# Kernel tuning notes

Measured on AMD Instinct MI355X. Metric: run time of the kernel, lower is better.

The kernel has to match this reference:

```python
import jax, jax.numpy as jnp
import numpy as np

TAU = 0.1
EPS = 1e-8  # torch CosineSimilarity eps


def _neg_indices(B):
    # static (numpy) column indices of the non-masked (negative) entries per row
    N = 2 * B
    mask = ~(np.eye(N, dtype=bool)
             | np.eye(N, k=B, dtype=bool)
             | np.eye(N, k=-B, dtype=bool))
    return np.where(mask)[1].reshape(N, N - 2)  # [2B, 2B-2]


def setup_inputs() -> dict:
    key = jax.random.key(0)
    k1, k2 = jax.random.split(key)
    zis = jax.random.normal(k1, (4096, 128), dtype=jnp.float32)
    zjs = jax.random.normal(k2, (4096, 128), dtype=jnp.float32)
    return {"zis": zis, "zjs": zjs}


def reference(zis, zjs):
    B = zis.shape[0]
    N = 2 * B
    reps = jnp.concatenate([zjs, zis], axis=0)  # [2B, D]
    # cosine similarity via normalize + GEMM
    norm = jnp.linalg.norm(reps, axis=-1, keepdims=True)
    rn = reps / jnp.maximum(norm, EPS)
    sim = rn @ rn.T  # [2B, 2B]

    l_pos = jnp.diagonal(sim, offset=B)   # [B]
    r_pos = jnp.diagonal(sim, offset=-B)  # [B]
    positives = jnp.concatenate([l_pos, r_pos])[:, None]  # [2B, 1]

    neg_idx = jnp.asarray(_neg_indices(B))  # static [2B, 2B-2]
    negatives = jnp.take_along_axis(sim, neg_idx, axis=1)  # [2B, 2B-2]

    logits = jnp.concatenate([positives, negatives], axis=1) / TAU  # [2B, 2B-1]
    logp = jax.nn.log_softmax(logits, axis=-1)
    # labels are all zeros; CrossEntropyLoss(reduction='sum')
    CE = -jnp.sum(logp[:, 0])
    # pt = mean over full [2B, 2B-1] of onehot * softmax = sum softmax[:,0] / (2B*(2B-1))
    pt = jnp.sum(jnp.exp(logp[:, 0])) / (N * (N - 1))
    epsilon = float(B)
    loss = CE / N + epsilon * (1.0 / B - pt)
    return loss
```

## Files before the change

kernel.cpp:

```cpp
#include <hip/hip_runtime.h>
#include <hip/hip_bf16.h>

#define BSZ 4096
#define NSZ 8192
#define DD  128
#define TILE 128
#define INV_TAU 10.0f
#define GROUPS 8
#define TPB 8

typedef __attribute__((ext_vector_type(8))) short bf16x8;
typedef __attribute__((ext_vector_type(4))) float f32x4;

typedef __attribute__((address_space(3))) unsigned int lds_u32;
typedef const __attribute__((address_space(1))) unsigned int glb_u32;

__global__ __launch_bounds__(256)
void norm_kernel(const float* __restrict__ zis,
                 const float* __restrict__ zjs,
                 __hip_bfloat16* __restrict__ rn) {
    const int row  = blockIdx.x * 4 + (threadIdx.x >> 6);
    const int lane = threadIdx.x & 63;
    const float* src = (row < BSZ) ? (zjs + (size_t)row * DD)
                                   : (zis + (size_t)(row - BSZ) * DD);
    float2 v = *(const float2*)(src + lane * 2);
    float ss = v.x * v.x + v.y * v.y;
    #pragma unroll
    for (int off = 32; off; off >>= 1) ss += __shfl_xor(ss, off);
    float inv = 1.0f / fmaxf(sqrtf(ss), 1e-8f);
    __hip_bfloat16 a = __float2bfloat16(v.x * inv);
    __hip_bfloat16 b = __float2bfloat16(v.y * inv);
    ushort2 pk;
    pk.x = *(const ushort*)&a;
    pk.y = *(const ushort*)&b;
    *(ushort2*)(rn + (size_t)row * DD + lane * 2) = pk;
}

__global__ __launch_bounds__(256, 2)
void sim_lse_kernel(const __hip_bfloat16* __restrict__ rn,
                    float* __restrict__ partials,
                    float* __restrict__ pos) {
    __shared__ ushort Bt[2][TILE * DD];

    const int g   = blockIdx.x;
    const int bi  = blockIdx.y;
    const int tid = threadIdx.x;
    const int wid  = tid >> 6;
    const int lane = tid & 63;
    const int l15  = lane & 15;
    const int kg   = lane >> 4;
    const int wm   = wid >> 1;
    const int wn   = wid & 1;

    const char* abase = (const char*)rn + (size_t)(bi * TILE + wm * 64 + l15) * 256;
    bf16x8 af[4][4];
    #pragma unroll
    for (int mf = 0; mf < 4; ++mf)
        #pragma unroll
        for (int kk = 0; kk < 4; ++kk)
            af[mf][kk] = *(const bf16x8*)(abase + mf * 16 * 256 + kk * 64 + kg * 16);

    {
        const char* gbase = (const char*)rn + (size_t)(g * TPB) * TILE * 256;
        #pragma unroll
        for (int j = 0; j < 8; ++j) {
            int cs  = (wid * 8 + j) * 64 + lane;
            int gsc = cs ^ ((cs >> 4) & 7);
            __builtin_amdgcn_global_load_lds((glb_u32*)(gbase + (size_t)gsc * 16),
                                             (lds_u32*)(&Bt[0][0] + (wid * 8 + j) * 512),
                                             16, 0, 0);
        }
    }
    __syncthreads();

    float rsum[4][4] = {};
    const int bjp = (bi + 32) & 63;

    for (int t = 0; t < TPB; ++t) {
        const int bj = g * TPB + t;

        if (t + 1 < TPB) {
            const char* gbase = (const char*)rn + (size_t)(bj + 1) * TILE * 256;
            ushort* dst = &Bt[(t + 1) & 1][0];
            #pragma unroll
            for (int j = 0; j < 8; ++j) {
                int cs  = (wid * 8 + j) * 64 + lane;
                int gsc = cs ^ ((cs >> 4) & 7);
                __builtin_amdgcn_global_load_lds((glb_u32*)(gbase + (size_t)gsc * 16),
                                                 (lds_u32*)(dst + (wid * 8 + j) * 512),
                                                 16, 0, 0);
            }
        }

        f32x4 acc[4][4] = {};
        const char* Bb = (const char*)&Bt[t & 1][0];
        #pragma unroll
        for (int kk = 0; kk < 4; ++kk) {
            const int kb = kk * 64 + kg * 16;
            bf16x8 bfr[4];
            #pragma unroll
            for (int nf = 0; nf < 4; ++nf) {
                int cR = wn * 64 + nf * 16 + l15;
                int o = cR * 256 + kb;
                bfr[nf] = *(const bf16x8*)(Bb + (o ^ ((cR & 7) << 4)));
            }
            #pragma unroll
            for (int mf = 0; mf < 4; ++mf)
                #pragma unroll
                for (int nf = 0; nf < 4; ++nf)
                    acc[mf][nf] = __builtin_amdgcn_mfma_f32_16x16x32_bf16(
                        af[mf][kk], bfr[nf], acc[mf][nf], 0, 0, 0);
        }

        const bool diag = (bj == bi);
        const bool posb = (bj == bjp) && (wm == wn);
        const bool dglb = diag && (wm == wn);
        #pragma unroll
        for (int mf = 0; mf < 4; ++mf) {
            #pragma unroll
            for (int nf = 0; nf < 4; ++nf) {
                #pragma unroll
                for (int reg = 0; reg < 4; ++reg) {
                    float s = acc[mf][nf][reg];
                    bool hit = (mf == nf) && ((kg * 4 + reg) == l15);
                    if (posb && hit)
                        pos[bi * TILE + wm * 64 + mf * 16 + l15] = s;
                    float p = __expf(s * INV_TAU);
                    if (dglb && hit) p = 0.0f;
                    rsum[mf][reg] += p;
                }
            }
        }

        __syncthreads();
    }

    #pragma unroll
    for (int mf = 0; mf < 4; ++mf)
        #pragma unroll
        for (int reg = 0; reg < 4; ++reg) {
            float v = rsum[mf][reg];
            v += __shfl_xor(v, 1);
            v += __shfl_xor(v, 2);
            v += __shfl_xor(v, 4);
            v += __shfl_xor(v, 8);
            rsum[mf][reg] = v;
        }

    float* red = (float*)&Bt[0][0];
    if (wn == 1 && l15 == 0) {
        #pragma unroll
        for (int mf = 0; mf < 4; ++mf)
            #pragma unroll
            for (int reg = 0; reg < 4; ++reg)
                red[wm * 64 + mf * 16 + kg * 4 + reg] = rsum[mf][reg];
    }
    __syncthreads();
    if (wn == 0 && l15 == 0) {
        #pragma unroll
        for (int mf = 0; mf < 4; ++mf)
            #pragma unroll
            for (int reg = 0; reg < 4; ++reg) {
                int lr = wm * 64 + mf * 16 + kg * 4 + reg;
                partials[(size_t)g * NSZ + bi * TILE + lr] = rsum[mf][reg] + red[lr];
            }
    }
}

__global__ __launch_bounds__(1024)
void reduce_kernel(const float* __restrict__ partials,
                   const float* __restrict__ pos,
                   float* __restrict__ out) {
    int tid = threadIdx.x;
    int base = tid * 8;
    float se[8] = {0.f, 0.f, 0.f, 0.f, 0.f, 0.f, 0.f, 0.f};
    #pragma unroll
    for (int gr = 0; gr < GROUPS; ++gr) {
        const float* p = partials + (size_t)gr * NSZ + base;
        float4 a = *(const float4*)(p);
        float4 b = *(const float4*)(p + 4);
        se[0] += a.x; se[1] += a.y; se[2] += a.z; se[3] += a.w;
        se[4] += b.x; se[5] += b.y; se[6] += b.z; se[7] += b.w;
    }
    float ce = 0.f, pt = 0.f;
    #pragma unroll
    for (int h = 0; h < 2; ++h) {
        float4 p4 = *(const float4*)(pos + base + h * 4);
        const float* pp = (const float*)&p4;
        #pragma unroll
        for (int q = 0; q < 4; ++q) {
            float s = se[h * 4 + q];
            ce += __logf(s) - pp[q] * INV_TAU;
            pt += __expf(pp[q] * INV_TAU) / s;
        }
    }
    #pragma unroll
    for (int off = 32; off; off >>= 1) {
        ce += __shfl_xor(ce, off);
        pt += __shfl_xor(pt, off);
    }
    __shared__ float lce[16], lpt[16];
    if ((tid & 63) == 0) { lce[tid >> 6] = ce; lpt[tid >> 6] = pt; }
    __syncthreads();
    if (tid == 0) {
        float CE = 0.f, PT = 0.f;
        #pragma unroll
        for (int w = 0; w < 16; ++w) { CE += lce[w]; PT += lpt[w]; }
        float loss = CE / (float)NSZ + 1.0f
                   - PT * ((float)BSZ / ((float)NSZ * (float)(NSZ - 1)));
        out[0] = loss;
    }
}

extern "C" void kernel_launch(void* const* d_in, const int* in_sizes, int n_in,
                              void* d_out, int out_size, void* d_ws, size_t ws_size,
                              hipStream_t stream) {
    const float* zis = (const float*)d_in[0];
    const float* zjs = (const float*)d_in[1];
    float* out = (float*)d_out;

    char* ws = (char*)d_ws;
    __hip_bfloat16* rn = (__hip_bfloat16*)ws;
    float* partials = (float*)(ws + 2 * 1024 * 1024);
    float* pos      = (float*)(ws + 2 * 1024 * 1024 + 256 * 1024);

    norm_kernel<<<NSZ / 4, 256, 0, stream>>>(zis, zjs, rn);

    dim3 grid(GROUPS, 64);
    sim_lse_kernel<<<grid, 256, 0, stream>>>(rn, partials, pos);

    reduce_kernel<<<1, 1024, 0, stream>>>(partials, pos, out);
}
```

Baseline: 40.94 us.

## Load B fragments directly from global memory, dropping LDS double buffering

The similarity kernel no longer stages B tiles through double-buffered LDS with global_load_lds and per-tile barriers. Each wave now reads its B fragments straight from global memory into registers, processing the N dimension in two halves to limit live accumulators, and the 2-blocks-per-CU launch bound is removed. Exponentials switch to exp2f with the 1/tau and log2(e) factors folded into one constant, and the self-similarity term is subtracted afterwards instead of masked per element. This trades the LDS traffic and barriers for duplicated global/L2 reads across waves, which adds some cancellation risk in the diagonal subtraction.

```diff
diff --git a/kernel.cpp b/kernel.cpp
--- a/kernel.cpp
+++ b/kernel.cpp
@@ -5,15 +5,12 @@
 #define NSZ 8192
 #define DD  128
 #define TILE 128
-#define INV_TAU 10.0f
 #define GROUPS 8
 #define TPB 8
+#define C2 14.426950408889634f
 
 typedef __attribute__((ext_vector_type(8))) short bf16x8;
 typedef __attribute__((ext_vector_type(4))) float f32x4;
-
-typedef __attribute__((address_space(3))) unsigned int lds_u32;
-typedef const __attribute__((address_space(1))) unsigned int glb_u32;
 
 __global__ __launch_bounds__(256)
 void norm_kernel(const float* __restrict__ zis,
@@ -36,12 +33,10 @@
     *(ushort2*)(rn + (size_t)row * DD + lane * 2) = pk;
 }
 
-__global__ __launch_bounds__(256, 2)
+__global__ __launch_bounds__(256)
 void sim_lse_kernel(const __hip_bfloat16* __restrict__ rn,
                     float* __restrict__ partials,
                     float* __restrict__ pos) {
-    __shared__ ushort Bt[2][TILE * DD];
-
     const int g   = blockIdx.x;
     const int bi  = blockIdx.y;
     const int tid = threadIdx.x;
@@ -60,81 +55,68 @@
         for (int kk = 0; kk < 4; ++kk)
             af[mf][kk] = *(const bf16x8*)(abase + mf * 16 * 256 + kk * 64 + kg * 16);
 
-    {
-        const char* gbase = (const char*)rn + (size_t)(g * TPB) * TILE * 256;
-        #pragma unroll
-        for (int j = 0; j < 8; ++j) {
-            int cs  = (wid * 8 + j) * 64 + lane;
-            int gsc = cs ^ ((cs >> 4) & 7);
-            __builtin_amdgcn_global_load_lds((glb_u32*)(gbase + (size_t)gsc * 16),
-                                             (lds_u32*)(&Bt[0][0] + (wid * 8 + j) * 512),
-                                             16, 0, 0);
-        }
-    }
-    __syncthreads();
-
     float rsum[4][4] = {};
     const int bjp = (bi + 32) & 63;
 
     for (int t = 0; t < TPB; ++t) {
         const int bj = g * TPB + t;
-
-        if (t + 1 < TPB) {
-            const char* gbase = (const char*)rn + (size_t)(bj + 1) * TILE * 256;
-            ushort* dst = &Bt[(t + 1) & 1][0];
-            #pragma unroll
-            for (int j = 0; j < 8; ++j) {
-                int cs  = (wid * 8 + j) * 64 + lane;
-                int gsc = cs ^ ((cs >> 4) & 7);
-                __builtin_amdgcn_global_load_lds((glb_u32*)(gbase + (size_t)gsc * 16),
-                                                 (lds_u32*)(dst + (wid * 8 + j) * 512),
-                                                 16, 0, 0);
+        const char* bbase = (const char*)rn
+                          + (size_t)bj * TILE * 256 + (size_t)(wn * 64) * 256;
+        const bool dglb = (bj == bi)  && (wm == wn);
+        const bool pglb = (bj == bjp) && (wm == wn);
+
+        #pragma unroll
+        for (int nh = 0; nh < 2; ++nh) {
+            bf16x8 bfr[2][4];
+            #pragma unroll
+            for (int nf2 = 0; nf2 < 2; ++nf2)
+                #pragma unroll
+                for (int kk = 0; kk < 4; ++kk)
+                    bfr[nf2][kk] = *(const bf16x8*)(bbase
+                        + (size_t)((nh * 2 + nf2) * 16 + l15) * 256 + kk * 64 + kg * 16);
+
+            f32x4 acc[4][2] = {};
+            #pragma unroll
+            for (int kk = 0; kk < 4; ++kk)
+                #pragma unroll
+                for (int mf = 0; mf < 4; ++mf)
+                    #pragma unroll
+                    for (int nf2 = 0; nf2 < 2; ++nf2)
+                        acc[mf][nf2] = __builtin_amdgcn_mfma_f32_16x16x32_bf16(
+                            af[mf][kk], bfr[nf2][kk], acc[mf][nf2], 0, 0, 0);
+
+            #pragma unroll
+            for (int mf = 0; mf < 4; ++mf)
+                #pragma unroll
+                for (int nf2 = 0; nf2 < 2; ++nf2)
+                    #pragma unroll
+                    for (int reg = 0; reg < 4; ++reg)
+                        rsum[mf][reg] += exp2f(acc[mf][nf2][reg] * C2);
+
+            if (dglb) {
+                #pragma unroll
+                for (int nf2 = 0; nf2 < 2; ++nf2) {
+                    const int mf = nh * 2 + nf2;
+                    #pragma unroll
+                    for (int reg = 0; reg < 4; ++reg)
+                        if (kg * 4 + reg == l15)
+                            rsum[mf][reg] -= exp2f(acc[mf][nf2][reg] * C2);
+                }
             }
-        }
-
-        f32x4 acc[4][4] = {};
-        const char* Bb = (const char*)&Bt[t & 1][0];
-        #pragma unroll
-        for (int kk = 0; kk < 4; ++kk) {
-            const int kb = kk * 64 + kg * 16;
-            bf16x8 bfr[4];
-            #pragma unroll
-            for (int nf = 0; nf < 4; ++nf) {
-                int cR = wn * 64 + nf * 16 + l15;
-                int o = cR * 256 + kb;
-                bfr[nf] = *(const bf16x8*)(Bb + (o ^ ((cR & 7) << 4)));
-            }
-            #pragma unroll
-            for (int mf = 0; mf < 4; ++mf)
-                #pragma unroll
-                for (int nf = 0; nf < 4; ++nf)
-                    acc[mf][nf] = __builtin_amdgcn_mfma_f32_16x16x32_bf16(
-                        af[mf][kk], bfr[nf], acc[mf][nf], 0, 0, 0);
-        }
-
-        const bool diag = (bj == bi);
-        const bool posb = (bj == bjp) && (wm == wn);
-        const bool dglb = diag && (wm == wn);
-        #pragma unroll
-        for (int mf = 0; mf < 4; ++mf) {
-            #pragma unroll
-            for (int nf = 0; nf < 4; ++nf) {
-                #pragma unroll
-                for (int reg = 0; reg < 4; ++reg) {
-                    float s = acc[mf][nf][reg];
-                    bool hit = (mf == nf) && ((kg * 4 + reg) == l15);
-                    if (posb && hit)
-                        pos[bi * TILE + wm * 64 + mf * 16 + l15] = s;
-                    float p = __expf(s * INV_TAU);
-                    if (dglb && hit) p = 0.0f;
-                    rsum[mf][reg] += p;
+            if (pglb) {
+                #pragma unroll
+                for (int nf2 = 0; nf2 < 2; ++nf2) {
+                    const int mf = nh * 2 + nf2;
+                    #pragma unroll
+                    for (int reg = 0; reg < 4; ++reg)
+                        if (kg * 4 + reg == l15)
+                            pos[bi * TILE + wm * 64 + mf * 16 + l15] = acc[mf][nf2][reg];
                 }
             }
         }
-
-        __syncthreads();
-    }
-
+    }
+
+    __shared__ float red[2][64];
     #pragma unroll
     for (int mf = 0; mf < 4; ++mf)
         #pragma unroll
@@ -146,14 +128,12 @@
             v += __shfl_xor(v, 8);
             rsum[mf][reg] = v;
         }
-
-    float* red = (float*)&Bt[0][0];
     if (wn == 1 && l15 == 0) {
         #pragma unroll
         for (int mf = 0; mf < 4; ++mf)
             #pragma unroll
             for (int reg = 0; reg < 4; ++reg)
-                red[wm * 64 + mf * 16 + kg * 4 + reg] = rsum[mf][reg];
+                red[wm][mf * 16 + kg * 4 + reg] = rsum[mf][reg];
     }
     __syncthreads();
     if (wn == 0 && l15 == 0) {
@@ -161,8 +141,9 @@
         for (int mf = 0; mf < 4; ++mf)
             #pragma unroll
             for (int reg = 0; reg < 4; ++reg) {
-                int lr = wm * 64 + mf * 16 + kg * 4 + reg;
-                partials[(size_t)g * NSZ + bi * TILE + lr] = rsum[mf][reg] + red[lr];
+                int lr = mf * 16 + kg * 4 + reg;
+                partials[(size_t)g * NSZ + bi * TILE + wm * 64 + lr] =
+                    rsum[mf][reg] + red[wm][lr];
             }
     }
 }
@@ -190,8 +171,8 @@
         #pragma unroll
         for (int q = 0; q < 4; ++q) {
             float s = se[h * 4 + q];
-            ce += __logf(s) - pp[q] * INV_TAU;
-            pt += __expf(pp[q] * INV_TAU) / s;
+            ce += __logf(s) - pp[q] * 10.0f;
+            pt += exp2f(pp[q] * C2) / s;
         }
     }
     #pragma unroll
```

Result: slower. 51.64 us (+26.1%).

## Exploit symmetry of similarity matrix to compute only half the tiles

Applied to the files above, without the earlier changes.

Uses the symmetry of the cosine-similarity matrix so each block computes only tile offsets 0..31 (plus offset 32 for half the rows), emitting both row sums and column sums per tile. Column partial sums go into extra partial buffers that the reduce kernel now sums over 70-72 slices. This roughly halves the MFMA and exp work in the main kernel. In exchange the reduce kernel reads much more data and runs as a single block, and each tile now does extra cross-lane shuffles and column-sum writes.

```diff
diff --git a/kernel.cpp b/kernel.cpp
--- a/kernel.cpp
+++ b/kernel.cpp
@@ -5,9 +5,6 @@
 #define NSZ 8192
 #define DD  128
 #define TILE 128
-#define INV_TAU 10.0f
-#define GROUPS 8
-#define TPB 8
 
 typedef __attribute__((ext_vector_type(8))) short bf16x8;
 typedef __attribute__((ext_vector_type(4))) float f32x4;
@@ -42,7 +39,7 @@
                     float* __restrict__ pos) {
     __shared__ ushort Bt[2][TILE * DD];
 
-    const int g   = blockIdx.x;
+    const int q   = blockIdx.x;
     const int bi  = blockIdx.y;
     const int tid = threadIdx.x;
     const int wid  = tid >> 6;
@@ -52,6 +49,8 @@
     const int wm   = wid >> 1;
     const int wn   = wid & 1;
 
+    const int nt = (bi < 32 && (bi & 7) == q) ? 5 : 4;
+
     const char* abase = (const char*)rn + (size_t)(bi * TILE + wm * 64 + l15) * 256;
     bf16x8 af[4][4];
     #pragma unroll
@@ -61,7 +60,7 @@
             af[mf][kk] = *(const bf16x8*)(abase + mf * 16 * 256 + kk * 64 + kg * 16);
 
     {
-        const char* gbase = (const char*)rn + (size_t)(g * TPB) * TILE * 256;
+        const char* gbase = (const char*)rn + (size_t)(((bi + q * 4) & 63)) * TILE * 256;
         #pragma unroll
         for (int j = 0; j < 8; ++j) {
             int cs  = (wid * 8 + j) * 64 + lane;
@@ -74,13 +73,15 @@
     __syncthreads();
 
     float rsum[4][4] = {};
-    const int bjp = (bi + 32) & 63;
-
-    for (int t = 0; t < TPB; ++t) {
-        const int bj = g * TPB + t;
-
-        if (t + 1 < TPB) {
-            const char* gbase = (const char*)rn + (size_t)(bj + 1) * TILE * 256;
+
+    for (int t = 0; t < nt; ++t) {
+        const int d  = (t < 4) ? q * 4 + t : 32;
+        const int bj = (bi + d) & 63;
+
+        if (t + 1 < nt) {
+            const int dn  = (t + 1 < 4) ? q * 4 + t + 1 : 32;
+            const int bjn = (bi + dn) & 63;
+            const char* gbase = (const char*)rn + (size_t)bjn * TILE * 256;
             ushort* dst = &Bt[(t + 1) & 1][0];
             #pragma unroll
             for (int j = 0; j < 8; ++j) {
@@ -112,9 +113,9 @@
                         af[mf][kk], bfr[nf], acc[mf][nf], 0, 0, 0);
         }
 
-        const bool diag = (bj == bi);
-        const bool posb = (bj == bjp) && (wm == wn);
-        const bool dglb = diag && (wm == wn);
+        const bool dglb = (d == 0)  && (wm == wn);
+        const bool pglb = (d == 32) && (wm == wn);
+        float csum[4] = {0.f, 0.f, 0.f, 0.f};
         #pragma unroll
         for (int mf = 0; mf < 4; ++mf) {
             #pragma unroll
@@ -122,13 +123,27 @@
                 #pragma unroll
                 for (int reg = 0; reg < 4; ++reg) {
                     float s = acc[mf][nf][reg];
-                    bool hit = (mf == nf) && ((kg * 4 + reg) == l15);
-                    if (posb && hit)
+                    bool hit = (mf == nf) && (kg * 4 + reg == l15);
+                    if (pglb && hit) {
                         pos[bi * TILE + wm * 64 + mf * 16 + l15] = s;
-                    float p = __expf(s * INV_TAU);
+                        pos[(bi + 32) * TILE + wm * 64 + mf * 16 + l15] = s;
+                    }
+                    float p = __expf(s * 10.0f);
                     if (dglb && hit) p = 0.0f;
                     rsum[mf][reg] += p;
+                    csum[nf] += p;
                 }
+            }
+        }
+
+        if (d != 0) {
+            float* cp = partials + (size_t)(8 + (d - 1) * 2 + wm) * NSZ + bj * TILE;
+            #pragma unroll
+            for (int nf = 0; nf < 4; ++nf) {
+                float v = csum[nf];
+                v += __shfl_xor(v, 16);
+                v += __shfl_xor(v, 32);
+                if (kg == 0) cp[wn * 64 + nf * 16 + l15] = v;
             }
         }
 
@@ -162,7 +177,7 @@
             #pragma unroll
             for (int reg = 0; reg < 4; ++reg) {
                 int lr = wm * 64 + mf * 16 + kg * 4 + reg;
-                partials[(size_t)g * NSZ + bi * TILE + lr] = rsum[mf][reg] + red[lr];
+                partials[(size_t)q * NSZ + bi * TILE + lr] = rsum[mf][reg] + red[lr];
             }
     }
 }
@@ -174,24 +189,33 @@
     int tid = threadIdx.x;
     int base = tid * 8;
     float se[8] = {0.f, 0.f, 0.f, 0.f, 0.f, 0.f, 0.f, 0.f};
-    #pragma unroll
-    for (int gr = 0; gr < GROUPS; ++gr) {
+    for (int gr = 0; gr < 70; ++gr) {
         const float* p = partials + (size_t)gr * NSZ + base;
         float4 a = *(const float4*)(p);
         float4 b = *(const float4*)(p + 4);
         se[0] += a.x; se[1] += a.y; se[2] += a.z; se[3] += a.w;
         se[4] += b.x; se[5] += b.y; se[6] += b.z; se[7] += b.w;
     }
+    if (base >= BSZ) {
+        #pragma unroll
+        for (int gr = 70; gr < 72; ++gr) {
+            const float* p = partials + (size_t)gr * NSZ + base;
+            float4 a = *(const float4*)(p);
+            float4 b = *(const float4*)(p + 4);
+            se[0] += a.x; se[1] += a.y; se[2] += a.z; se[3] += a.w;
+            se[4] += b.x; se[5] += b.y; se[6] += b.z; se[7] += b.w;
+        }
+    }
     float ce = 0.f, pt = 0.f;
     #pragma unroll
     for (int h = 0; h < 2; ++h) {
         float4 p4 = *(const float4*)(pos + base + h * 4);
         const float* pp = (const float*)&p4;
         #pragma unroll
-        for (int q = 0; q < 4; ++q) {
-            float s = se[h * 4 + q];
-            ce += __logf(s) - pp[q] * INV_TAU;
-            pt += __expf(pp[q] * INV_TAU) / s;
+        for (int qq = 0; qq < 4; ++qq) {
+            float s = se[h * 4 + qq];
+            ce += __logf(s) - pp[qq] * 10.0f;
+            pt += __expf(pp[qq] * 10.0f) / s;
         }
     }
     #pragma unroll
@@ -222,11 +246,11 @@
     char* ws = (char*)d_ws;
     __hip_bfloat16* rn = (__hip_bfloat16*)ws;
     float* partials = (float*)(ws + 2 * 1024 * 1024);
-    float* pos      = (float*)(ws + 2 * 1024 * 1024 + 256 * 1024);
+    float* pos      = (float*)(ws + 2 * 1024 * 1024 + 72 * NSZ * 4);
 
     norm_kernel<<<NSZ / 4, 256, 0, stream>>>(zis, zjs, rn);
 
-    dim3 grid(GROUPS, 64);
+    dim3 grid(8, 64);
     sim_lse_kernel<<<grid, 256, 0, stream>>>(rn, partials, pos);
 
     reduce_kernel<<<1, 1024, 0, stream>>>(partials, pos, out);
```

After: 86.56 us. +111.4%, slower.

## Use 8 waves per block with 32-row tiles and drop LDS row reduction

Applied to the files above, without the earlier changes.

Moves the similarity/LSE kernel from 256 to 512 threads per block. Each wave now owns a 32x64 output sub-tile instead of 64x64, which halves the register-held A fragments and accumulators and spreads the tile loads over more waves. The cross-wave LDS reduction and its barrier are removed. Each wave instead writes its row sums to a separate partial slot, which doubles the partial buffer and the work in the final reduce kernel. This aims to raise latency hiding and occupancy, at the cost of more partial-buffer traffic and smaller per-wave MFMA work.

```diff
diff --git a/kernel.cpp b/kernel.cpp
--- a/kernel.cpp
+++ b/kernel.cpp
@@ -5,7 +5,6 @@
 #define NSZ 8192
 #define DD  128
 #define TILE 128
-#define INV_TAU 10.0f
 #define GROUPS 8
 #define TPB 8
 
@@ -36,7 +35,7 @@
     *(ushort2*)(rn + (size_t)row * DD + lane * 2) = pk;
 }
 
-__global__ __launch_bounds__(256, 2)
+__global__ __launch_bounds__(512)
 void sim_lse_kernel(const __hip_bfloat16* __restrict__ rn,
                     float* __restrict__ partials,
                     float* __restrict__ pos) {
@@ -52,10 +51,10 @@
     const int wm   = wid >> 1;
     const int wn   = wid & 1;
 
-    const char* abase = (const char*)rn + (size_t)(bi * TILE + wm * 64 + l15) * 256;
-    bf16x8 af[4][4];
-    #pragma unroll
-    for (int mf = 0; mf < 4; ++mf)
+    const char* abase = (const char*)rn + (size_t)(bi * TILE + wm * 32 + l15) * 256;
+    bf16x8 af[2][4];
+    #pragma unroll
+    for (int mf = 0; mf < 2; ++mf)
         #pragma unroll
         for (int kk = 0; kk < 4; ++kk)
             af[mf][kk] = *(const bf16x8*)(abase + mf * 16 * 256 + kk * 64 + kg * 16);
@@ -63,18 +62,20 @@
     {
         const char* gbase = (const char*)rn + (size_t)(g * TPB) * TILE * 256;
         #pragma unroll
-        for (int j = 0; j < 8; ++j) {
-            int cs  = (wid * 8 + j) * 64 + lane;
+        for (int j = 0; j < 4; ++j) {
+            int cs  = (wid * 4 + j) * 64 + lane;
             int gsc = cs ^ ((cs >> 4) & 7);
             __builtin_amdgcn_global_load_lds((glb_u32*)(gbase + (size_t)gsc * 16),
-                                             (lds_u32*)(&Bt[0][0] + (wid * 8 + j) * 512),
+                                             (lds_u32*)(&Bt[0][0] + (wid * 4 + j) * 512),
                                              16, 0, 0);
         }
     }
     __syncthreads();
 
-    float rsum[4][4] = {};
+    float rsum[2][4] = {};
     const int bjp = (bi + 32) & 63;
+    const int nfd = (wm & 1) * 2;
+    const bool wdiag = (wn == (wm >> 1));
 
     for (int t = 0; t < TPB; ++t) {
         const int bj = g * TPB + t;
@@ -83,16 +84,16 @@
             const char* gbase = (const char*)rn + (size_t)(bj + 1) * TILE * 256;
             ushort* dst = &Bt[(t + 1) & 1][0];
             #pragma unroll
-            for (int j = 0; j < 8; ++j) {
-                int cs  = (wid * 8 + j) * 64 + lane;
+            for (int j = 0; j < 4; ++j) {
+                int cs  = (wid * 4 + j) * 64 + lane;
                 int gsc = cs ^ ((cs >> 4) & 7);
                 __builtin_amdgcn_global_load_lds((glb_u32*)(gbase + (size_t)gsc * 16),
-                                                 (lds_u32*)(dst + (wid * 8 + j) * 512),
+                                                 (lds_u32*)(dst + (wid * 4 + j) * 512),
                                                  16, 0, 0);
             }
         }
 
-        f32x4 acc[4][4] = {};
+        f32x4 acc[2][4] = {};
         const char* Bb = (const char*)&Bt[t & 1][0];
         #pragma unroll
         for (int kk = 0; kk < 4; ++kk) {
@@ -105,27 +106,26 @@
                 bfr[nf] = *(const bf16x8*)(Bb + (o ^ ((cR & 7) << 4)));
             }
             #pragma unroll
-            for (int mf = 0; mf < 4; ++mf)
+            for (int mf = 0; mf < 2; ++mf)
                 #pragma unroll
                 for (int nf = 0; nf < 4; ++nf)
                     acc[mf][nf] = __builtin_amdgcn_mfma_f32_16x16x32_bf16(
                         af[mf][kk], bfr[nf], acc[mf][nf], 0, 0, 0);
         }
 
-        const bool diag = (bj == bi);
-        const bool posb = (bj == bjp) && (wm == wn);
-        const bool dglb = diag && (wm == wn);
-        #pragma unroll
-        for (int mf = 0; mf < 4; ++mf) {
+        const bool dglb = (bj == bi)  && wdiag;
+        const bool pglb = (bj == bjp) && wdiag;
+        #pragma unroll
+        for (int mf = 0; mf < 2; ++mf) {
             #pragma unroll
             for (int nf = 0; nf < 4; ++nf) {
                 #pragma unroll
                 for (int reg = 0; reg < 4; ++reg) {
                     float s = acc[mf][nf][reg];
-                    bool hit = (mf == nf) && ((kg * 4 + reg) == l15);
-                    if (posb && hit)
-                        pos[bi * TILE + wm * 64 + mf * 16 + l15] = s;
-                    float p = __expf(s * INV_TAU);
+                    bool hit = (nf == nfd + mf) && (kg * 4 + reg == l15);
+                    if (pglb && hit)
+                        pos[bi * TILE + wm * 32 + mf * 16 + l15] = s;
+                    float p = __expf(s * 10.0f);
                     if (dglb && hit) p = 0.0f;
                     rsum[mf][reg] += p;
                 }
@@ -136,7 +136,7 @@
     }
 
     #pragma unroll
-    for (int mf = 0; mf < 4; ++mf)
+    for (int mf = 0; mf < 2; ++mf)
         #pragma unroll
         for (int reg = 0; reg < 4; ++reg) {
             float v = rsum[mf][reg];
@@ -144,27 +144,10 @@
             v += __shfl_xor(v, 2);
             v += __shfl_xor(v, 4);
             v += __shfl_xor(v, 8);
-            rsum[mf][reg] = v;
-        }
-
-    float* red = (float*)&Bt[0][0];
-    if (wn == 1 && l15 == 0) {
-        #pragma unroll
-        for (int mf = 0; mf < 4; ++mf)
-            #pragma unroll
-            for (int reg = 0; reg < 4; ++reg)
-                red[wm * 64 + mf * 16 + kg * 4 + reg] = rsum[mf][reg];
-    }
-    __syncthreads();
-    if (wn == 0 && l15 == 0) {
-        #pragma unroll
-        for (int mf = 0; mf < 4; ++mf)
-            #pragma unroll
-            for (int reg = 0; reg < 4; ++reg) {
-                int lr = wm * 64 + mf * 16 + kg * 4 + reg;
-                partials[(size_t)g * NSZ + bi * TILE + lr] = rsum[mf][reg] + red[lr];
-            }
-    }
+            if (l15 == 0)
+                partials[(size_t)(g * 2 + wn) * NSZ
+                         + bi * TILE + wm * 32 + mf * 16 + kg * 4 + reg] = v;
+        }
 }
 
 __global__ __launch_bounds__(1024)
@@ -175,7 +158,7 @@
     int base = tid * 8;
     float se[8] = {0.f, 0.f, 0.f, 0.f, 0.f, 0.f, 0.f, 0.f};
     #pragma unroll
-    for (int gr = 0; gr < GROUPS; ++gr) {
+    for (int gr = 0; gr < 2 * GROUPS; ++gr) {
         const float* p = partials + (size_t)gr * NSZ + base;
         float4 a = *(const float4*)(p);
         float4 b = *(const float4*)(p + 4);
@@ -190,8 +173,8 @@
         #pragma unroll
         for (int q = 0; q < 4; ++q) {
             float s = se[h * 4 + q];
-            ce += __logf(s) - pp[q] * INV_TAU;
-            pt += __expf(pp[q] * INV_TAU) / s;
+            ce += __logf(s) - pp[q] * 10.0f;
+            pt += __expf(pp[q] * 10.0f) / s;
         }
     }
     #pragma unroll
@@ -222,12 +205,12 @@
     char* ws = (char*)d_ws;
     __hip_bfloat16* rn = (__hip_bfloat16*)ws;
     float* partials = (float*)(ws + 2 * 1024 * 1024);
-    float* pos      = (float*)(ws + 2 * 1024 * 1024 + 256 * 1024);
+    float* pos      = (float*)(ws + 2 * 1024 * 1024 + 512 * 1024);
 
     norm_kernel<<<NSZ / 4, 256, 0, stream>>>(zis, zjs, rn);
 
     dim3 grid(GROUPS, 64);
-    sim_lse_kernel<<<grid, 256, 0, stream>>>(rn, partials, pos);
+    sim_lse_kernel<<<grid, 512, 0, stream>>>(rn, partials, pos);
 
     reduce_kernel<<<1, 1024, 0, stream>>>(partials, pos, out);
 }
```

After: 46.22 us. 1.13x slower.
